# Kernel optimization log

Hardware: AMD Instinct MI355X
Metric: run time of the kernel (lower is better)

The kernel has to match this reference:

```python
import jax, jax.numpy as jnp
import numpy as np

TOP_K = 4


def setup_inputs() -> dict:
    key = jax.random.key(0)
    k1, k2, k3 = jax.random.split(key, 3)
    T, H, E = 16384, 2880, 128
    hidden_states = jax.random.normal(k1, (T, H), dtype=jnp.float32)
    weight = jax.random.normal(k2, (E, H), dtype=jnp.float32) * 0.02
    bias = jax.random.normal(k3, (E,), dtype=jnp.float32) * 0.02
    return {"hidden_states": hidden_states, "weight": weight, "bias": bias}


def reference(hidden_states, weight, bias):
    # [T, H] @ [H, E] + [E] -> router logits [T, E]
    hidden_states = hidden_states.reshape(-1, weight.shape[1])
    router_logits = jnp.einsum('th,eh->te', hidden_states, weight) + bias
    # top-k over experts, then softmax over the k selected logits
    router_top_value, router_indices = jax.lax.top_k(router_logits, TOP_K)
    router_scores = jax.nn.softmax(router_top_value, axis=-1)
    return router_scores, router_indices
```

## Files before the change

kernel.cpp:

```cpp
#include <hip/hip_runtime.h>
#include <hip/hip_bf16.h>
#include <math.h>

#define T_TOKENS 16384
#define H_DIM    2880
#define KHALF    1440
#define E_EXP    128
#define TOPK     4
#define MT       32
#define MTM      64
#define KC       32
#define NCHUNK   (H_DIM / KC)
#define NCHUNK_H (KHALF / KC)
#define EPS_GAP  5e-4f

#define WS_WOFF   64
#define WS_WBYTES (NCHUNK * 1024 * 16)
#define WS_FLOFF  (WS_WOFF + WS_WBYTES)
#define WS_CAOFF  (WS_FLOFF + T_TOKENS * 4)
#define WS_NEED   (WS_CAOFF + T_TOKENS * 8)

typedef __bf16 bf16x8 __attribute__((ext_vector_type(8)));
typedef float  f32x4  __attribute__((ext_vector_type(4)));

__device__ __forceinline__ void split2(float a, float b,
                                       unsigned int& hi, unsigned int& lo) {
    float2 p; p.x = a; p.y = b;
    __hip_bfloat162 h = __float22bfloat162_rn(p);
    unsigned int hu; __builtin_memcpy(&hu, &h, 4);
    float2 r;
    r.x = a - __uint_as_float((hu & 0xffffu) << 16);
    r.y = b - __uint_as_float(hu & 0xffff0000u);
    __hip_bfloat162 l = __float22bfloat162_rn(r);
    unsigned int lu; __builtin_memcpy(&lu, &l, 4);
    hi = hu; lo = lu;
}

__global__ __launch_bounds__(256) void prep_w(const float* __restrict__ W,
                                              uint4* __restrict__ wsW) {
    const int f   = blockIdx.x * 256 + threadIdx.x;
    const int kc  = f >> 9;
    const int rem = f & 511;
    const int nt  = rem >> 6;
    const int L   = rem & 63;
    const int e   = nt * 16 + (L & 15);
    const int k   = kc * KC + (L >> 4) * 8;
    const float* p = W + (size_t)e * H_DIM + k;
    const float4 x0 = *(const float4*)p;
    const float4 x1 = *(const float4*)(p + 4);
    uint4 hi, lo;
    split2(x0.x, x0.y, hi.x, lo.x);
    split2(x0.z, x0.w, hi.y, lo.y);
    split2(x1.x, x1.y, hi.z, lo.z);
    split2(x1.z, x1.w, hi.w, lo.w);
    wsW[(size_t)kc * 1024 + nt * 64 + L]       = hi;
    wsW[(size_t)kc * 1024 + 512 + nt * 64 + L] = lo;
}

__global__ __launch_bounds__(1024, 4) void router_main(
    const float* __restrict__ A, const uint4* __restrict__ wsW,
    const float* __restrict__ bias, float* __restrict__ out,
    int* __restrict__ flag_count, int* __restrict__ flag_list,
    uint2* __restrict__ cand_list)
{
    union SMem {
        struct {
            uint4 W  [2][2][1024];
            uint4 Ahi[2][2][4][64];
            uint4 Alo[2][2][4][64];
        } s;
        float L[MTM][129];
    };
    __shared__ SMem sm;

    const int tid    = threadIdx.x;
    const int t_base = blockIdx.x * MTM;

    const int wave  = tid >> 6;
    const int L     = tid & 63;
    const int whalf = wave >> 3;
    const int wmg   = (wave >> 2) & 1;
    const int wng   = wave & 3;

    const int shalf = whalf;
    const int wv    = wave & 7;
    const uint4* wsrc = wsW + (size_t)(shalf * NCHUNK_H) * 1024 + (wv * 2) * 64 + L;

    const int at   = tid >> 4;
    const int kq   = tid & 15;
    const int ah   = kq >> 3;
    const int oct  = (kq >> 1) & 3;
    const int sub  = kq & 1;
    const int amt  = at >> 4;
    const int t16  = at & 15;
    const float* Ag = A + (size_t)(t_base + at) * H_DIM + ah * KHALF + oct * 8 + sub * 4;

    f32x4 acc[2][2];
#pragma unroll
    for (int m = 0; m < 2; ++m)
#pragma unroll
        for (int n = 0; n < 2; ++n) { f32x4 z = {0.f, 0.f, 0.f, 0.f}; acc[m][n] = z; }

#define GLDS(SRC, DST) \
    __builtin_amdgcn_global_load_lds( \
        (const __attribute__((address_space(1))) void*)(SRC), \
        (__attribute__((address_space(3))) void*)(DST), 16, 0, 0)

#define STAGE_W(NB, IT)                                                        \
    {                                                                          \
        const uint4* wc = wsrc + (size_t)(IT) * 1024;                          \
        GLDS(wc,      &sm.s.W[NB][shalf][(wv * 2 + 0) * 64]);                  \
        GLDS(wc + 64, &sm.s.W[NB][shalf][(wv * 2 + 1) * 64]);                  \
    }

#define STAGE_A(NB)                                                            \
    {                                                                          \
        uint2 h2, l2;                                                          \
        split2(av.x, av.y, h2.x, l2.x);                                        \
        split2(av.z, av.w, h2.y, l2.y);                                        \
        ((uint2*)&sm.s.Ahi[NB][ah][amt][oct * 16 + t16])[sub] = h2;            \
        ((uint2*)&sm.s.Alo[NB][ah][amt][oct * 16 + t16])[sub] = l2;            \
    }

#define COMPUTE(NB)                                                            \
    {                                                                          \
        const bf16x8 ah0 = *(const bf16x8*)&sm.s.Ahi[NB][whalf][wmg * 2 + 0][L]; \
        const bf16x8 al0 = *(const bf16x8*)&sm.s.Alo[NB][whalf][wmg * 2 + 0][L]; \
        const bf16x8 ah1 = *(const bf16x8*)&sm.s.Ahi[NB][whalf][wmg * 2 + 1][L]; \
        const bf16x8 al1 = *(const bf16x8*)&sm.s.Alo[NB][whalf][wmg * 2 + 1][L]; \
        _Pragma("unroll")                                                      \
        for (int n = 0; n < 2; ++n) {                                          \
            const int nt = wng * 2 + n;                                        \
            const bf16x8 whi = *(const bf16x8*)&sm.s.W[NB][whalf][nt * 64 + L]; \
            const bf16x8 wlo = *(const bf16x8*)&sm.s.W[NB][whalf][512 + nt * 64 + L]; \
            acc[0][n] = __builtin_amdgcn_mfma_f32_16x16x32_bf16(ah0, whi, acc[0][n], 0, 0, 0); \
            acc[0][n] = __builtin_amdgcn_mfma_f32_16x16x32_bf16(ah0, wlo, acc[0][n], 0, 0, 0); \
            acc[0][n] = __builtin_amdgcn_mfma_f32_16x16x32_bf16(al0, whi, acc[0][n], 0, 0, 0); \
            acc[1][n] = __builtin_amdgcn_mfma_f32_16x16x32_bf16(ah1, whi, acc[1][n], 0, 0, 0); \
            acc[1][n] = __builtin_amdgcn_mfma_f32_16x16x32_bf16(ah1, wlo, acc[1][n], 0, 0, 0); \
            acc[1][n] = __builtin_amdgcn_mfma_f32_16x16x32_bf16(al1, whi, acc[1][n], 0, 0, 0); \
        }                                                                      \
    }

#define CBAR(VM)                                                               \
    asm volatile("s_waitcnt vmcnt(" #VM ") lgkmcnt(0)" ::: "memory");          \
    __builtin_amdgcn_s_barrier();                                              \
    __builtin_amdgcn_sched_barrier(0);

    float4 av = *(const float4*)Ag;
    STAGE_A(0);
    STAGE_W(0, 0);
    __builtin_amdgcn_sched_barrier(0);
    av = *(const float4*)(Ag + KC);
    CBAR(1)

    int b = 0;
    for (int it = 0; it < NCHUNK_H - 2; ++it) {
        STAGE_W(b ^ 1, it + 1);
        __builtin_amdgcn_sched_barrier(0);
        const float4 avn = *(const float4*)(Ag + (it + 2) * KC);
        STAGE_A(b ^ 1);
        av = avn;
        COMPUTE(b);
        CBAR(1)
        b ^= 1;
    }
    {
        STAGE_W(b ^ 1, NCHUNK_H - 1);
        STAGE_A(b ^ 1);
        COMPUTE(b);
        CBAR(0)
        b ^= 1;
    }
    COMPUTE(b);
    __syncthreads();

#undef GLDS
#undef STAGE_W
#undef STAGE_A
#undef COMPUTE
#undef CBAR

    if (whalf == 0) {
#pragma unroll
        for (int m = 0; m < 2; ++m)
#pragma unroll
            for (int n = 0; n < 2; ++n) {
                const int e = (wng * 2 + n) * 16 + (L & 15);
                const float bv = bias[e];
#pragma unroll
                for (int r = 0; r < 4; ++r)
                    sm.L[(wmg * 2 + m) * 16 + (L >> 4) * 4 + r][e] = acc[m][n][r] + bv;
            }
    }
    __syncthreads();
    if (whalf == 1) {
#pragma unroll
        for (int m = 0; m < 2; ++m)
#pragma unroll
            for (int n = 0; n < 2; ++n) {
                const int e = (wng * 2 + n) * 16 + (L & 15);
#pragma unroll
                for (int r = 0; r < 4; ++r)
                    sm.L[(wmg * 2 + m) * 16 + (L >> 4) * 4 + r][e] += acc[m][n][r];
            }
    }
    __syncthreads();

    if (tid < MTM) {
        float v0 = -1e30f, v1 = -1e30f, v2 = -1e30f, v3 = -1e30f, v4 = -1e30f;
        int   i0 = 0, i1 = 0, i2 = 0, i3 = 0, i4 = 0;
        for (int e = 0; e < E_EXP; ++e) {
            const float x = sm.L[tid][e];
            if (x > v4) {
                if (x > v0)      { v4=v3;i4=i3; v3=v2;i3=i2; v2=v1;i2=i1; v1=v0;i1=i0; v0=x;i0=e; }
                else if (x > v1) { v4=v3;i4=i3; v3=v2;i3=i2; v2=v1;i2=i1; v1=x;i1=e; }
                else if (x > v2) { v4=v3;i4=i3; v3=v2;i3=i2; v2=x;i2=e; }
                else if (x > v3) { v4=v3;i4=i3; v3=x;i3=e; }
                else             { v4=x;i4=e; }
            }
        }
        const float g0 = v0 - v1, g1 = v1 - v2, g2 = v2 - v3, g3 = v3 - v4;
        float mg = g0 < g1 ? g0 : g1;
        mg = mg < g2 ? mg : g2;
        mg = mg < g3 ? mg : g3;

        const float e0x = expf(v0 - v0);
        const float e1x = expf(v1 - v0);
        const float e2x = expf(v2 - v0);
        const float e3x = expf(v3 - v0);
        const float s   = e0x + e1x + e2x + e3x;

        const int gt = t_base + tid;
        float* out_scores = out;
        float* out_idx    = out + (size_t)T_TOKENS * TOPK;
        out_scores[gt * 4 + 0] = e0x / s;
        out_scores[gt * 4 + 1] = e1x / s;
        out_scores[gt * 4 + 2] = e2x / s;
        out_scores[gt * 4 + 3] = e3x / s;
        out_idx[gt * 4 + 0] = (float)i0;
        out_idx[gt * 4 + 1] = (float)i1;
        out_idx[gt * 4 + 2] = (float)i2;
        out_idx[gt * 4 + 3] = (float)i3;

        if (mg < EPS_GAP) {
            const int p = atomicAdd(flag_count, 1);
            if (p < T_TOKENS) {
                flag_list[p] = gt;
                unsigned ids[8];
                int nc = 0;
                const float thr = v3 - EPS_GAP;
                for (int e = 0; e < E_EXP; ++e) {
                    if (sm.L[tid][e] >= thr) {
                        if (nc < 8) ids[nc] = (unsigned)e;
                        ++nc;
                    }
                }
                uint2 cd;
                if (nc > 8) {
                    cd.x = 0xFEu; cd.y = 0xFFFFFFFFu;
                } else {
                    for (int q = nc; q < 8; ++q) ids[q] = 0xFFu;
                    cd.x = ids[0] | (ids[1] << 8) | (ids[2] << 16) | (ids[3] << 24);
                    cd.y = ids[4] | (ids[5] << 8) | (ids[6] << 16) | (ids[7] << 24);
                }
                cand_list[p] = cd;
            }
        }
    }
}

__global__ __launch_bounds__(256) void router_recheck(
    const float* __restrict__ A, const float* __restrict__ W,
    const float* __restrict__ bias, float* __restrict__ out,
    const int* __restrict__ flag_count, const int* __restrict__ flag_list,
    const uint2* __restrict__ cand_list)
{
    __shared__ float  sA[H_DIM];
    __shared__ double sLog[8];
    __shared__ int    sIds[8];
    __shared__ double sPart[256];
    __shared__ double sFull[E_EXP];

    int count = *flag_count;
    if (count > T_TOKENS) count = T_TOKENS;

    const int tid = threadIdx.x;

    for (int i = blockIdx.x; i < count; i += gridDim.x) {
        const int t = flag_list[i];
        const uint2 cd = cand_list[i];
        __syncthreads();

        for (int q = tid; q < H_DIM / 4; q += 256)
            *(float4*)&sA[q * 4] = *(const float4*)(A + (size_t)t * H_DIM + q * 4);
        __syncthreads();

        const bool full = ((cd.x & 0xFFu) == 0xFEu);
        if (!full) {
            const int sl = tid >> 5;
            const int j  = tid & 31;
            const unsigned e = (sl < 4 ? (cd.x >> (sl * 8)) : (cd.y >> ((sl - 4) * 8))) & 0xFFu;
            double sum = 0.0;
            if (e < E_EXP) {
                const float* wrow = W + (size_t)e * H_DIM;
                for (int k = j; k < H_DIM; k += 32)
                    sum += (double)sA[k] * (double)wrow[k];
            }
#pragma unroll
            for (int off = 16; off > 0; off >>= 1)
                sum += __shfl_down(sum, off, 32);
            if (j == 0) {
                sIds[sl] = (e < E_EXP) ? (int)e : -1;
                sLog[sl] = (e < E_EXP) ? (sum + (double)bias[e]) : -1e300;
            }
            __syncthreads();
            if (tid == 0) {
                double v0 = -1e300, v1 = -1e300, v2 = -1e300, v3 = -1e300;
                int    i0 = 0, i1 = 0, i2 = 0, i3 = 0;
                for (int q = 0; q < 8; ++q) {
                    if (sIds[q] < 0) continue;
                    const double x = sLog[q];
                    const int    id = sIds[q];
                    if (x > v3) {
                        if (x > v0)      { v3=v2;i3=i2; v2=v1;i2=i1; v1=v0;i1=i0; v0=x;i0=id; }
                        else if (x > v1) { v3=v2;i3=i2; v2=v1;i2=i1; v1=x;i1=id; }
                        else if (x > v2) { v3=v2;i3=i2; v2=x;i2=id; }
                        else             { v3=x;i3=id; }
                    }
                }
                const double e0x = exp(v0 - v0);
                const double e1x = exp(v1 - v0);
                const double e2x = exp(v2 - v0);
                const double e3x = exp(v3 - v0);
                const double s   = e0x + e1x + e2x + e3x;
                float* out_scores = out;
                float* out_idx    = out + (size_t)T_TOKENS * TOPK;
                out_scores[t * 4 + 0] = (float)(e0x / s);
                out_scores[t * 4 + 1] = (float)(e1x / s);
                out_scores[t * 4 + 2] = (float)(e2x / s);
                out_scores[t * 4 + 3] = (float)(e3x / s);
                out_idx[t * 4 + 0] = (float)i0;
                out_idx[t * 4 + 1] = (float)i1;
                out_idx[t * 4 + 2] = (float)i2;
                out_idx[t * 4 + 3] = (float)i3;
            }
        } else {
            const int e = tid & (E_EXP - 1);
            const int h = tid >> 7;
            const float* wrow = W + (size_t)e * H_DIM + h * KHALF;
            const float* arow = &sA[h * KHALF];
            double s0 = 0.0, s1 = 0.0;
            for (int k = 0; k < KHALF; k += 2) {
                s0 += (double)arow[k]     * (double)wrow[k];
                s1 += (double)arow[k + 1] * (double)wrow[k + 1];
            }
            sPart[tid] = s0 + s1;
            __syncthreads();
            if (h == 0) sFull[e] = sPart[e] + sPart[e + 128] + (double)bias[e];
            __syncthreads();
            if (tid == 0) {
                double v0 = -1e300, v1 = -1e300, v2 = -1e300, v3 = -1e300;
                int    i0 = 0, i1 = 0, i2 = 0, i3 = 0;
                for (int q = 0; q < E_EXP; ++q) {
                    const double x = sFull[q];
                    if (x > v3) {
                        if (x > v0)      { v3=v2;i3=i2; v2=v1;i2=i1; v1=v0;i1=i0; v0=x;i0=q; }
                        else if (x > v1) { v3=v2;i3=i2; v2=v1;i2=i1; v1=x;i1=q; }
                        else if (x > v2) { v3=v2;i3=i2; v2=x;i2=q; }
                        else             { v3=x;i3=q; }
                    }
                }
                const double e0x = exp(v0 - v0);
                const double e1x = exp(v1 - v0);
                const double e2x = exp(v2 - v0);
                const double e3x = exp(v3 - v0);
                const double s   = e0x + e1x + e2x + e3x;
                float* out_scores = out;
                float* out_idx    = out + (size_t)T_TOKENS * TOPK;
                out_scores[t * 4 + 0] = (float)(e0x / s);
                out_scores[t * 4 + 1] = (float)(e1x / s);
                out_scores[t * 4 + 2] = (float)(e2x / s);
                out_scores[t * 4 + 3] = (float)(e3x / s);
                out_idx[t * 4 + 0] = (float)i0;
                out_idx[t * 4 + 1] = (float)i1;
                out_idx[t * 4 + 2] = (float)i2;
                out_idx[t * 4 + 3] = (float)i3;
            }
        }
        __syncthreads();
    }
}

__global__ __launch_bounds__(512, 4) void router_main_fb(
    const float* __restrict__ A, const float* __restrict__ W,
    const float* __restrict__ bias, float* __restrict__ out,
    int* __restrict__ flag_count, int* __restrict__ flag_list)
{
    __shared__ __align__(16) uint2 sAhi[2][2][128];
    __shared__ __align__(16) uint2 sAlo[2][2][128];
    __shared__ __align__(16) uint4 sWhi[2][8][64];
    __shared__ __align__(16) uint4 sWlo[2][8][64];
    __shared__ float sL[MT][129];

    const int tid    = threadIdx.x;
    const int t_base = blockIdx.x * MT;
    const int wave  = tid >> 6;
    const int L     = tid & 63;
    const int whalf = wave >> 2;
    const int wm    = wave & 1;
    const int wn    = (wave >> 1) & 1;
    const int shalf = tid >> 8;
    const int tid_h = tid & 255;
    const int at = tid_h >> 3;
    const int ac = tid_h & 7;
    const int a_idx = (at >> 4) * 128 + ((((ac >> 1) << 4) | (at & 15)) << 1) + (ac & 1);
    const float* Ag = A + (size_t)(t_base + at) * H_DIM + shalf * KHALF + ac * 4;
    const int we  = tid_h >> 1;
    const int wq0 = (tid_h & 1) * 2;
    const float* Wg = W + (size_t)we * H_DIM + shalf * KHALF + wq0 * 8;
    const int w_nt = we >> 4;
    const int w_n  = we & 15;

    uint2* sAhiF = &sAhi[shalf][0][0];
    uint2* sAloF = &sAlo[shalf][0][0];

    f32x4 acc[4];
#pragma unroll
    for (int i = 0; i < 4; ++i) { f32x4 z = {0.f, 0.f, 0.f, 0.f}; acc[i] = z; }

    for (int k0 = 0; k0 < KHALF; k0 += KC) {
        const float4 av  = *(const float4*)(Ag + k0);
        const float4 wv0 = *(const float4*)(Wg + k0);
        const float4 wv1 = *(const float4*)(Wg + k0 + 4);
        const float4 wv2 = *(const float4*)(Wg + k0 + 8);
        const float4 wv3 = *(const float4*)(Wg + k0 + 12);

        uint2 ahp, alp;
        split2(av.x, av.y, ahp.x, alp.x);
        split2(av.z, av.w, ahp.y, alp.y);
        uint4 whp0, wlp0, whp1, wlp1;
        split2(wv0.x, wv0.y, whp0.x, wlp0.x);
        split2(wv0.z, wv0.w, whp0.y, wlp0.y);
        split2(wv1.x, wv1.y, whp0.z, wlp0.z);
        split2(wv1.z, wv1.w, whp0.w, wlp0.w);
        split2(wv2.x, wv2.y, whp1.x, wlp1.x);
        split2(wv2.z, wv2.w, whp1.y, wlp1.y);
        split2(wv3.x, wv3.y, whp1.z, wlp1.z);
        split2(wv3.z, wv3.w, whp1.w, wlp1.w);

        __syncthreads();
        sAhiF[a_idx] = ahp;
        sAloF[a_idx] = alp;
        sWhi[shalf][w_nt][((wq0 + 0) << 4) | w_n] = whp0;
        sWhi[shalf][w_nt][((wq0 + 1) << 4) | w_n] = whp1;
        sWlo[shalf][w_nt][((wq0 + 0) << 4) | w_n] = wlp0;
        sWlo[shalf][w_nt][((wq0 + 1) << 4) | w_n] = wlp1;
        __syncthreads();

        const bf16x8 ahi = *(const bf16x8*)&sAhi[whalf][wm][L * 2];
        const bf16x8 alo = *(const bf16x8*)&sAlo[whalf][wm][L * 2];
#pragma unroll
        for (int i = 0; i < 4; ++i) {
            const int nt = wn * 4 + i;
            const bf16x8 whi = *(const bf16x8*)&sWhi[whalf][nt][L];
            const bf16x8 wlo = *(const bf16x8*)&sWlo[whalf][nt][L];
            acc[i] = __builtin_amdgcn_mfma_f32_16x16x32_bf16(ahi, whi, acc[i], 0, 0, 0);
            acc[i] = __builtin_amdgcn_mfma_f32_16x16x32_bf16(ahi, wlo, acc[i], 0, 0, 0);
            acc[i] = __builtin_amdgcn_mfma_f32_16x16x32_bf16(alo, whi, acc[i], 0, 0, 0);
        }
    }

    __syncthreads();
    if (whalf == 0) {
#pragma unroll
        for (int i = 0; i < 4; ++i) {
            const int e = wn * 64 + i * 16 + (L & 15);
            const float b = bias[e];
#pragma unroll
            for (int r = 0; r < 4; ++r)
                sL[wm * 16 + (L >> 4) * 4 + r][e] = acc[i][r] + b;
        }
    }
    __syncthreads();
    if (whalf == 1) {
#pragma unroll
        for (int i = 0; i < 4; ++i) {
            const int e = wn * 64 + i * 16 + (L & 15);
#pragma unroll
            for (int r = 0; r < 4; ++r)
                sL[wm * 16 + (L >> 4) * 4 + r][e] += acc[i][r];
        }
    }
    __syncthreads();

    if (tid < MT) {
        float v0 = -1e30f, v1 = -1e30f, v2 = -1e30f, v3 = -1e30f, v4 = -1e30f;
        int   i0 = 0, i1 = 0, i2 = 0, i3 = 0, i4 = 0;
        for (int e = 0; e < E_EXP; ++e) {
            const float x = sL[tid][e];
            if (x > v4) {
                if (x > v0)      { v4=v3;i4=i3; v3=v2;i3=i2; v2=v1;i2=i1; v1=v0;i1=i0; v0=x;i0=e; }
                else if (x > v1) { v4=v3;i4=i3; v3=v2;i3=i2; v2=v1;i2=i1; v1=x;i1=e; }
                else if (x > v2) { v4=v3;i4=i3; v3=v2;i3=i2; v2=x;i2=e; }
                else if (x > v3) { v4=v3;i4=i3; v3=x;i3=e; }
                else             { v4=x;i4=e; }
            }
        }
        const float g0 = v0 - v1, g1 = v1 - v2, g2 = v2 - v3, g3 = v3 - v4;
        float mg = g0 < g1 ? g0 : g1;
        mg = mg < g2 ? mg : g2;
        mg = mg < g3 ? mg : g3;

        const float e0x = expf(v0 - v0);
        const float e1x = expf(v1 - v0);
        const float e2x = expf(v2 - v0);
        const float e3x = expf(v3 - v0);
        const float s   = e0x + e1x + e2x + e3x;

        const int gt = t_base + tid;
        float* out_scores = out;
        float* out_idx    = out + (size_t)T_TOKENS * TOPK;
        out_scores[gt * 4 + 0] = e0x / s;
        out_scores[gt * 4 + 1] = e1x / s;
        out_scores[gt * 4 + 2] = e2x / s;
        out_scores[gt * 4 + 3] = e3x / s;
        out_idx[gt * 4 + 0] = (float)i0;
        out_idx[gt * 4 + 1] = (float)i1;
        out_idx[gt * 4 + 2] = (float)i2;
        out_idx[gt * 4 + 3] = (float)i3;

        if (mg < EPS_GAP) {
            const int p = atomicAdd(flag_count, 1);
            if (p < T_TOKENS) flag_list[p] = gt;
        }
    }
}

__global__ __launch_bounds__(256) void router_recheck_fb(
    const float* __restrict__ A, const float* __restrict__ W,
    const float* __restrict__ bias, float* __restrict__ out,
    const int* __restrict__ flag_count, const int* __restrict__ flag_list)
{
    __shared__ double sPart[256];
    __shared__ double sLog[E_EXP];

    int count = *flag_count;
    if (count > T_TOKENS) count = T_TOKENS;

    const int tid = threadIdx.x;
    const int e   = tid & (E_EXP - 1);
    const int h   = tid >> 7;

    for (int i = blockIdx.x; i < count; i += gridDim.x) {
        const int t = flag_list[i];
        const float* arow = A + (size_t)t * H_DIM + h * KHALF;
        const float* wrow = W + (size_t)e * H_DIM + h * KHALF;

        double s0 = 0.0, s1 = 0.0, s2 = 0.0, s3 = 0.0;
        float4 a[8], w[8];
#pragma unroll
        for (int q = 0; q < 8; ++q) {
            a[q] = *(const float4*)(arow + q * 4);
            w[q] = *(const float4*)(wrow + q * 4);
        }
        for (int it = 0; it < KHALF / 32 - 1; ++it) {
            const float* ap = arow + (it + 1) * 32;
            const float* wp = wrow + (it + 1) * 32;
            float4 na[8], nw[8];
#pragma unroll
            for (int q = 0; q < 8; ++q) {
                na[q] = *(const float4*)(ap + q * 4);
                nw[q] = *(const float4*)(wp + q * 4);
            }
#pragma unroll
            for (int q = 0; q < 8; ++q) {
                s0 += (double)a[q].x * (double)w[q].x;
                s1 += (double)a[q].y * (double)w[q].y;
                s2 += (double)a[q].z * (double)w[q].z;
                s3 += (double)a[q].w * (double)w[q].w;
            }
#pragma unroll
            for (int q = 0; q < 8; ++q) { a[q] = na[q]; w[q] = nw[q]; }
        }
#pragma unroll
        for (int q = 0; q < 8; ++q) {
            s0 += (double)a[q].x * (double)w[q].x;
            s1 += (double)a[q].y * (double)w[q].y;
            s2 += (double)a[q].z * (double)w[q].z;
            s3 += (double)a[q].w * (double)w[q].w;
        }
        sPart[tid] = (s0 + s1) + (s2 + s3);
        __syncthreads();
        if (h == 0) sLog[e] = sPart[e] + sPart[e + 128] + (double)bias[e];
        __syncthreads();

        if (tid == 0) {
            double v0 = -1e300, v1 = -1e300, v2 = -1e300, v3 = -1e300;
            int    i0 = 0, i1 = 0, i2 = 0, i3 = 0;
            for (int q = 0; q < E_EXP; ++q) {
                const double x = sLog[q];
                if (x > v3) {
                    if (x > v0)      { v3=v2;i3=i2; v2=v1;i2=i1; v1=v0;i1=i0; v0=x;i0=q; }
                    else if (x > v1) { v3=v2;i3=i2; v2=v1;i2=i1; v1=x;i1=q; }
                    else if (x > v2) { v3=v2;i3=i2; v2=x;i2=q; }
                    else             { v3=x;i3=q; }
                }
            }
            const double e0x = exp(v0 - v0);
            const double e1x = exp(v1 - v0);
            const double e2x = exp(v2 - v0);
            const double e3x = exp(v3 - v0);
            const double s   = e0x + e1x + e2x + e3x;
            float* out_scores = out;
            float* out_idx    = out + (size_t)T_TOKENS * TOPK;
            out_scores[t * 4 + 0] = (float)(e0x / s);
            out_scores[t * 4 + 1] = (float)(e1x / s);
            out_scores[t * 4 + 2] = (float)(e2x / s);
            out_scores[t * 4 + 3] = (float)(e3x / s);
            out_idx[t * 4 + 0] = (float)i0;
            out_idx[t * 4 + 1] = (float)i1;
            out_idx[t * 4 + 2] = (float)i2;
            out_idx[t * 4 + 3] = (float)i3;
        }
        __syncthreads();
    }
}

extern "C" void kernel_launch(void* const* d_in, const int* in_sizes, int n_in,
                              void* d_out, int out_size, void* d_ws, size_t ws_size,
                              hipStream_t stream) {
    const float* A    = (const float*)d_in[0];
    const float* W    = (const float*)d_in[1];
    const float* bias = (const float*)d_in[2];
    float* out = (float*)d_out;

    if (ws_size >= (size_t)WS_NEED) {
        int*   flag_count = (int*)d_ws;
        uint4* wsW        = (uint4*)((char*)d_ws + WS_WOFF);
        int*   flag_list  = (int*)((char*)d_ws + WS_FLOFF);
        uint2* cand_list  = (uint2*)((char*)d_ws + WS_CAOFF);
        hipMemsetAsync(flag_count, 0, sizeof(int), stream);
        prep_w<<<dim3((NCHUNK * 512) / 256), dim3(256), 0, stream>>>(W, wsW);
        router_main<<<dim3(T_TOKENS / MTM), dim3(1024), 0, stream>>>(
            A, wsW, bias, out, flag_count, flag_list, cand_list);
        router_recheck<<<dim3(512), dim3(256), 0, stream>>>(
            A, W, bias, out, flag_count, flag_list, cand_list);
    } else {
        int* flag_count = (int*)d_ws;
        int* flag_list  = (int*)d_ws + 1;
        hipMemsetAsync(flag_count, 0, sizeof(int), stream);
        router_main_fb<<<dim3(T_TOKENS / MT), dim3(512), 0, stream>>>(A, W, bias, out,
                                                                      flag_count, flag_list);
        router_recheck_fb<<<dim3(512), dim3(256), 0, stream>>>(A, W, bias, out,
                                                               flag_count, flag_list);
    }
}
```

Before: 344.2 us.

## Triple-buffer weight chunks in LDS and XOR-swizzle activation tile slots

Weight chunks move from double to triple buffering in LDS, so each chunk is prefetched two iterations ahead. The barrier wait now leaves more global-to-LDS loads in flight (vmcnt 3 instead of 1), which should hide more global memory latency. Activation hi/lo slots in LDS are XOR-swizzled by octet and K-half, with reads de-swizzled to match, to cut LDS bank conflicts. LDS use grows by 32 KB per block, which could limit occupancy or how the compiler schedules the loop.

```diff
diff --git a/kernel.cpp b/kernel.cpp
--- a/kernel.cpp
+++ b/kernel.cpp
@@ -65,7 +65,7 @@
 {
     union SMem {
         struct {
-            uint4 W  [2][2][1024];
+            uint4 W  [3][2][1024];
             uint4 Ahi[2][2][4][64];
             uint4 Alo[2][2][4][64];
         } s;
@@ -93,7 +93,10 @@
     const int sub  = kq & 1;
     const int amt  = at >> 4;
     const int t16  = at & 15;
+    const int aL   = oct * 16 + (t16 ^ (oct << 1) ^ ah);
     const float* Ag = A + (size_t)(t_base + at) * H_DIM + ah * KHALF + oct * 8 + sub * 4;
+
+    const int aslot = L ^ ((L >> 4) << 1) ^ whalf;
 
     f32x4 acc[2][2];
 #pragma unroll
@@ -106,11 +109,11 @@
         (const __attribute__((address_space(1))) void*)(SRC), \
         (__attribute__((address_space(3))) void*)(DST), 16, 0, 0)
 
-#define STAGE_W(NB, IT)                                                        \
+#define STAGE_W(WB, IT)                                                        \
     {                                                                          \
         const uint4* wc = wsrc + (size_t)(IT) * 1024;                          \
-        GLDS(wc,      &sm.s.W[NB][shalf][(wv * 2 + 0) * 64]);                  \
-        GLDS(wc + 64, &sm.s.W[NB][shalf][(wv * 2 + 1) * 64]);                  \
+        GLDS(wc,      &sm.s.W[WB][shalf][(wv * 2 + 0) * 64]);                  \
+        GLDS(wc + 64, &sm.s.W[WB][shalf][(wv * 2 + 1) * 64]);                  \
     }
 
 #define STAGE_A(NB)                                                            \
@@ -118,21 +121,21 @@
         uint2 h2, l2;                                                          \
         split2(av.x, av.y, h2.x, l2.x);                                        \
         split2(av.z, av.w, h2.y, l2.y);                                        \
-        ((uint2*)&sm.s.Ahi[NB][ah][amt][oct * 16 + t16])[sub] = h2;            \
-        ((uint2*)&sm.s.Alo[NB][ah][amt][oct * 16 + t16])[sub] = l2;            \
-    }
-
-#define COMPUTE(NB)                                                            \
+        ((uint2*)&sm.s.Ahi[NB][ah][amt][aL])[sub] = h2;                        \
+        ((uint2*)&sm.s.Alo[NB][ah][amt][aL])[sub] = l2;                        \
+    }
+
+#define COMPUTE(WB, AB)                                                        \
     {                                                                          \
-        const bf16x8 ah0 = *(const bf16x8*)&sm.s.Ahi[NB][whalf][wmg * 2 + 0][L]; \
-        const bf16x8 al0 = *(const bf16x8*)&sm.s.Alo[NB][whalf][wmg * 2 + 0][L]; \
-        const bf16x8 ah1 = *(const bf16x8*)&sm.s.Ahi[NB][whalf][wmg * 2 + 1][L]; \
-        const bf16x8 al1 = *(const bf16x8*)&sm.s.Alo[NB][whalf][wmg * 2 + 1][L]; \
+        const bf16x8 ah0 = *(const bf16x8*)&sm.s.Ahi[AB][whalf][wmg * 2 + 0][aslot]; \
+        const bf16x8 al0 = *(const bf16x8*)&sm.s.Alo[AB][whalf][wmg * 2 + 0][aslot]; \
+        const bf16x8 ah1 = *(const bf16x8*)&sm.s.Ahi[AB][whalf][wmg * 2 + 1][aslot]; \
+        const bf16x8 al1 = *(const bf16x8*)&sm.s.Alo[AB][whalf][wmg * 2 + 1][aslot]; \
         _Pragma("unroll")                                                      \
         for (int n = 0; n < 2; ++n) {                                          \
             const int nt = wng * 2 + n;                                        \
-            const bf16x8 whi = *(const bf16x8*)&sm.s.W[NB][whalf][nt * 64 + L]; \
-            const bf16x8 wlo = *(const bf16x8*)&sm.s.W[NB][whalf][512 + nt * 64 + L]; \
+            const bf16x8 whi = *(const bf16x8*)&sm.s.W[WB][whalf][nt * 64 + L]; \
+            const bf16x8 wlo = *(const bf16x8*)&sm.s.W[WB][whalf][512 + nt * 64 + L]; \
             acc[0][n] = __builtin_amdgcn_mfma_f32_16x16x32_bf16(ah0, whi, acc[0][n], 0, 0, 0); \
             acc[0][n] = __builtin_amdgcn_mfma_f32_16x16x32_bf16(ah0, wlo, acc[0][n], 0, 0, 0); \
             acc[0][n] = __builtin_amdgcn_mfma_f32_16x16x32_bf16(al0, whi, acc[0][n], 0, 0, 0); \
@@ -152,27 +155,33 @@
     STAGE_W(0, 0);
     __builtin_amdgcn_sched_barrier(0);
     av = *(const float4*)(Ag + KC);
-    CBAR(1)
+    __builtin_amdgcn_sched_barrier(0);
+    STAGE_W(1, 1);
+    __builtin_amdgcn_sched_barrier(0);
+    CBAR(3)
 
     int b = 0;
+    int wc_ = 0, wn_ = 1, ws_ = 2;
     for (int it = 0; it < NCHUNK_H - 2; ++it) {
-        STAGE_W(b ^ 1, it + 1);
+        const float4 avn = *(const float4*)(Ag + (it + 2) * KC);
         __builtin_amdgcn_sched_barrier(0);
-        const float4 avn = *(const float4*)(Ag + (it + 2) * KC);
+        STAGE_W(ws_, it + 2);
+        __builtin_amdgcn_sched_barrier(0);
         STAGE_A(b ^ 1);
         av = avn;
-        COMPUTE(b);
-        CBAR(1)
+        COMPUTE(wc_, b);
+        CBAR(3)
         b ^= 1;
+        const int t_ = wc_; wc_ = wn_; wn_ = ws_; ws_ = t_;
     }
     {
-        STAGE_W(b ^ 1, NCHUNK_H - 1);
         STAGE_A(b ^ 1);
-        COMPUTE(b);
+        COMPUTE(wc_, b);
         CBAR(0)
         b ^= 1;
-    }
-    COMPUTE(b);
+        const int t_ = wc_; wc_ = wn_; wn_ = ws_; ws_ = t_;
+    }
+    COMPUTE(wc_, b);
     __syncthreads();
 
 #undef GLDS
```

Result: no change. 349.6 us (+1.6%).
